# Optimization experiments

Hardware: AMD Instinct MI355X
Metric: run time of the kernel (lower is better)

## Reference

```python
import jax, jax.numpy as jnp
import numpy as np

B, T = 64, 20          # batch, caption length
C, HW = 512, 196       # cnn_channels, width*height (14x14)
V, E, U = 10000, 256, 512  # n_tokens, emb_size, lstm_units
MAX_NORM = 5.0


def setup_inputs() -> dict:
    key = jax.random.key(0)
    ks = jax.random.split(key, 12)
    s = 0.02
    return {
        "image_features": jax.random.normal(ks[0], (B, C, HW), jnp.float32),
        "captions_ix": jax.random.randint(ks[1], (B, T), 0, V, dtype=jnp.int32),
        "W_h0": jax.random.normal(ks[2], (U, C), jnp.float32) * s,
        "b_h0": jnp.zeros((U,), jnp.float32),
        "W_c0": jax.random.normal(ks[3], (U, C), jnp.float32) * s,
        "b_c0": jnp.zeros((U,), jnp.float32),
        "emb": jax.random.normal(ks[4], (V, E), jnp.float32) * s,
        "W_key": jax.random.normal(ks[5], (U, C), jnp.float32) * s,
        "b_key": jnp.zeros((U,), jnp.float32),
        "W_ih": jax.random.normal(ks[6], (4 * U, C + E), jnp.float32) * s,
        "b_ih": jnp.zeros((4 * U,), jnp.float32),
        "W_hh": jax.random.normal(ks[7], (4 * U, U), jnp.float32) * s,
        "b_hh": jnp.zeros((4 * U,), jnp.float32),
        "W_out": jax.random.normal(ks[8], (V, C + E + U), jnp.float32) * s,
        "b_out": jnp.zeros((V,), jnp.float32),
    }


def _caption_net(image_features, captions_ix, W_h0, b_h0, W_c0, b_c0, emb,
                 W_key, b_key, W_ih, b_ih, W_hh, b_hh, W_out, b_out):
    feats_mean = image_features.mean(axis=2)                # [B, C]
    hid0 = feats_mean @ W_h0.T + b_h0                       # [B, U]
    cell0 = feats_mean @ W_c0.T + b_c0                      # [B, U]
    feats = jnp.transpose(image_features, (0, 2, 1))        # [B, HW, C]
    keys = feats @ W_key.T + b_key                          # [B, HW, U]

    # nn.Embedding(max_norm=5): renorm rows whose L2 norm exceeds 5
    norms = jnp.linalg.norm(emb, axis=1, keepdims=True)
    emb_eff = emb * jnp.minimum(1.0, MAX_NORM / jnp.maximum(norms, 1e-12))
    cap_emb = emb_eff[captions_ix]                          # [B, T, E]

    inv_scale = 1.0 / (keys.shape[2] ** 0.5)

    def step(carry, emb_t):
        hid, cell = carry
        # scaled dot-product attention, query = current hidden state
        scores = jnp.einsum('bu,bku->bk', hid, keys) * inv_scale   # [B, HW]
        w = jax.nn.softmax(scores, axis=1)
        a = jnp.einsum('bk,bkc->bc', w, feats)                     # [B, C]
        x = jnp.concatenate([emb_t, a], axis=1)                    # [B, E+C]
        gates = x @ W_ih.T + b_ih + hid @ W_hh.T + b_hh            # [B, 4U]
        i, f, g, o = jnp.split(gates, 4, axis=1)
        cell = jax.nn.sigmoid(f) * cell + jax.nn.sigmoid(i) * jnp.tanh(g)
        hid = jax.nn.sigmoid(o) * jnp.tanh(cell)
        out = jnp.concatenate([hid, a, emb_t], axis=1)             # [B, U+C+E]
        return (hid, cell), (out, w)

    (_, _), (outs, attn) = jax.lax.scan(step, (hid0, cell0),
                                        jnp.transpose(cap_emb, (1, 0, 2)))
    outs = jnp.transpose(outs, (1, 0, 2))                   # [B, T, U+C+E]
    attn = jnp.transpose(attn, (1, 0, 2))                   # [B, T, HW]
    logits = outs @ W_out.T + b_out                         # [B, T, V]
    return logits, attn


def reference(image_features, captions_ix, W_h0, b_h0, W_c0, b_c0, emb,
              W_key, b_key, W_ih, b_ih, W_hh, b_hh, W_out, b_out):
    return _caption_net(image_features, captions_ix, W_h0, b_h0, W_c0, b_c0,
                        emb, W_key, b_key, W_ih, b_ih, W_hh, b_hh, W_out, b_out)
```

## Files before the change

kernel.cpp:

```cpp
#include <hip/hip_runtime.h>
#include <math.h>

#define B 64
#define T 20
#define C 512
#define HW 196
#define V 10000
#define E 256
#define U 512
#define G4U 2048
#define ODIM 1280
#define KTOT 1280
#define NBLK 64

typedef short bf8_t __attribute__((ext_vector_type(8)));
typedef float f4_t  __attribute__((ext_vector_type(4)));

__device__ __forceinline__ unsigned short f2bf(float f) {
    unsigned int u = __float_as_uint(f);
    return (unsigned short)((u + 0x7fffu + ((u >> 16) & 1u)) >> 16);
}
__device__ __forceinline__ float bf2f(unsigned short s) {
    return __uint_as_float((unsigned int)s << 16);
}
__device__ __forceinline__ float bflo(unsigned int kv) { return __uint_as_float(kv << 16); }
__device__ __forceinline__ float bfhi(unsigned int kv) { return __uint_as_float(kv & 0xffff0000u); }

__device__ __forceinline__ void coh_load4x2(const void* p0, const void* p1,
                                            uint4& r0, uint4& r1) {
    asm volatile("global_load_dwordx4 %0, %2, off sc0 sc1\n\t"
                 "global_load_dwordx4 %1, %3, off sc0 sc1\n\t"
                 "s_waitcnt vmcnt(0)"
                 : "=&v"(r0), "=&v"(r1) : "v"(p0), "v"(p1) : "memory");
}
__device__ __forceinline__ void coh_load4_issue(const void* p, uint4& r) {
    asm volatile("global_load_dwordx4 %0, %1, off sc0 sc1"
                 : "=&v"(r) : "v"(p) : "memory");
}
__device__ __forceinline__ void wait_vm0() {
    asm volatile("s_waitcnt vmcnt(0)" ::: "memory");
    __builtin_amdgcn_sched_barrier(0);
}
__device__ __forceinline__ void coh_store1f(void* p, float v) {
    asm volatile("global_store_dword %0, %1, off sc0 sc1" :: "v"(p), "v"(v) : "memory");
}
__device__ __forceinline__ void coh_store1u(void* p, unsigned int v) {
    asm volatile("global_store_dword %0, %1, off sc0 sc1" :: "v"(p), "v"(v) : "memory");
}
__device__ __forceinline__ void coh_store_us(void* p, unsigned int v) {
    asm volatile("global_store_short %0, %1, off sc0 sc1" :: "v"(p), "v"(v) : "memory");
}
__device__ __forceinline__ int coh_load_int(const int* p) {
    int v;
    asm volatile("global_load_dword %0, %1, off sc0 sc1\n\t"
                 "s_waitcnt vmcnt(0)"
                 : "=v"(v) : "v"(p) : "memory");
    return v;
}
__device__ __forceinline__ void coh_store_int(int* p, int v) {
    asm volatile("global_store_dword %0, %1, off sc0 sc1" :: "v"(p), "v"(v) : "memory");
}

__device__ __forceinline__ void gbarf(int* barf, int e) {
    asm volatile("s_waitcnt vmcnt(0)" ::: "memory");
    __syncthreads();
    int tid = threadIdx.x;
    if (blockIdx.x == 0) {
        if (tid == 0) coh_store_int(barf + 16, e);
        if (tid < 64) {
            while (!__all(coh_load_int(barf + 16 + tid * 16) >= e)) {}
            if (tid == 0) coh_store_int(barf, e);
        }
    } else {
        if (tid == 0) {
            coh_store_int(barf + 16 + blockIdx.x * 16, e);
            while (coh_load_int(barf) < e) {}
        }
    }
    __syncthreads();
}

__global__ void k_mean(const float* __restrict__ img, float* __restrict__ fm) {
    int wave = threadIdx.x >> 6;
    int lane = threadIdx.x & 63;
    int row = blockIdx.x * 4 + wave;
    const float* p = img + (size_t)row * HW;
    float s = p[lane] + p[lane + 64] + p[lane + 128];
    if (lane < 4) s += p[lane + 192];
    for (int off = 32; off > 0; off >>= 1) s += __shfl_down(s, off, 64);
    if (lane == 0) fm[row] = s * (1.0f / HW);
}

__global__ void k_init(const float* __restrict__ fm,
                       const float* __restrict__ W_h0, const float* __restrict__ b_h0,
                       const float* __restrict__ W_c0, const float* __restrict__ b_c0,
                       unsigned short* __restrict__ xb, float* __restrict__ cell) {
    int wv = blockIdx.x * 4 + (threadIdx.x >> 6);
    int lane = threadIdx.x & 63;
    int which = wv >> 15;
    int r = wv & 32767;
    int b = r >> 9, u = r & 511;
    const float* W = which ? W_c0 : W_h0;
    const float* bias = which ? b_c0 : b_h0;
    const float* f = fm + b * C;
    const float* w = W + (size_t)u * C;
    float s = 0.f;
    #pragma unroll
    for (int c = 0; c < C; c += 64) s += f[c + lane] * w[c + lane];
    for (int off = 32; off > 0; off >>= 1) s += __shfl_down(s, off, 64);
    if (lane == 0) {
        float v = s + bias[u];
        if (which) cell[r] = v;
        else       xb[(size_t)b * KTOT + 768 + u] = f2bf(v);
    }
}

__global__ void k_wkt(const float* __restrict__ Wk, float* __restrict__ WkT) {
    __shared__ float tile[64][65];
    int u0 = blockIdx.x * 64, c0 = blockIdx.y * 64;
    int x = threadIdx.x & 63, y0 = threadIdx.x >> 6;
    #pragma unroll
    for (int i = 0; i < 16; i++) {
        int r = y0 * 16 + i;
        tile[r][x] = Wk[(size_t)(u0 + r) * C + c0 + x];
    }
    __syncthreads();
    #pragma unroll
    for (int i = 0; i < 16; i++) {
        int r = y0 * 16 + i;
        WkT[(size_t)(c0 + r) * U + u0 + x] = tile[x][r];
    }
}

__global__ __launch_bounds__(256) void k_keys(const float* __restrict__ img,
        const float* __restrict__ WkT, const float* __restrict__ b_key,
        unsigned short* __restrict__ keys2) {
    __shared__ unsigned short st[32][200];
    int b = blockIdx.x >> 4;
    int u0 = (blockIdx.x & 15) * 32;
    int wave = __builtin_amdgcn_readfirstlane(threadIdx.x >> 6);
    int lane = threadIdx.x & 63;
    int lk = lane < 49 ? lane : 48;
    const f4_t* imgb = (const f4_t*)(img + (size_t)b * C * HW);
    f4_t acc[8];
    #pragma unroll
    for (int j = 0; j < 8; j++) acc[j] = (f4_t){0.f, 0.f, 0.f, 0.f};
    const float* wp = WkT + u0 + wave * 8;
    for (int c = 0; c < C; c++) {
        f4_t v = imgb[c * 49 + lk];
        const float* w = wp + (size_t)c * U;
        #pragma unroll
        for (int j = 0; j < 8; j++) acc[j] += v * w[j];
    }
    if (lane < 49) {
        #pragma unroll
        for (int j = 0; j < 8; j++) {
            float bk = b_key[u0 + wave * 8 + j];
            int ul = wave * 8 + j;
            int k = lane * 4;
            st[ul][k + 0] = f2bf(acc[j].x + bk);
            st[ul][k + 1] = f2bf(acc[j].y + bk);
            st[ul][k + 2] = f2bf(acc[j].z + bk);
            st[ul][k + 3] = f2bf(acc[j].w + bk);
        }
    }
    __syncthreads();
    int ui = threadIdx.x & 15;
    int kr = threadIdx.x >> 4;
    #pragma unroll
    for (int pass = 0; pass < 13; pass++) {
        int k = pass * 16 + kr;
        if (k < HW) {
            unsigned int lo = st[ui * 2][k];
            unsigned int hi = st[ui * 2 + 1][k];
            *(unsigned int*)&keys2[((size_t)b * HW + k) * U + u0 + ui * 2] = (hi << 16) | lo;
        }
    }
}

__global__ void k_wg(const float* __restrict__ W_ih, const float* __restrict__ W_hh,
                     unsigned short* __restrict__ Wg) {
    int j = blockIdx.x;
    int tid = threadIdx.x;
    const float* s1 = W_ih + (size_t)j * 768;
    const float* s2 = W_hh + (size_t)j * 512;
    unsigned short* dst = Wg + (size_t)j * KTOT;
    #pragma unroll
    for (int p = 0; p < 3; p++) dst[tid + p * 256] = f2bf(s1[tid + p * 256]);
    #pragma unroll
    for (int p = 0; p < 2; p++) dst[768 + tid + p * 256] = f2bf(s2[tid + p * 256]);
}

__global__ void k_emb(const int* __restrict__ ix, const float* __restrict__ emb,
                      unsigned short* __restrict__ outs, int* __restrict__ barf) {
    int bt = blockIdx.x;
    int e = threadIdx.x;
    if (bt == 0) {
        for (int i = e; i < 1040; i += 256) barf[i] = 0;
    }
    int row = ix[bt];
    float v = emb[(size_t)row * E + e];
    __shared__ float red[4];
    float sq = v * v;
    for (int off = 32; off > 0; off >>= 1) sq += __shfl_down(sq, off, 64);
    int wave = e >> 6, lane = e & 63;
    if (lane == 0) red[wave] = sq;
    __syncthreads();
    float norm = sqrtf(red[0] + red[1] + red[2] + red[3]);
    float scale = fminf(1.0f, 5.0f / fmaxf(norm, 1e-12f));
    outs[(size_t)bt * ODIM + (U + C) + e] = f2bf(v * scale);
}

__global__ __launch_bounds__(256) void k_wo(const float* __restrict__ W,
                                            unsigned short* __restrict__ Wb) {
    size_t i = ((size_t)blockIdx.x * 256 + threadIdx.x) * 8;
    float4 f0 = *(const float4*)(W + i);
    float4 f1 = *(const float4*)(W + i + 4);
    uint4 q;
    q.x = ((unsigned int)f2bf(f0.y) << 16) | f2bf(f0.x);
    q.y = ((unsigned int)f2bf(f0.w) << 16) | f2bf(f0.z);
    q.z = ((unsigned int)f2bf(f1.y) << 16) | f2bf(f1.x);
    q.w = ((unsigned int)f2bf(f1.w) << 16) | f2bf(f1.z);
    *(uint4*)(Wb + i) = q;
}

__global__ __launch_bounds__(256) void k_loop(
    unsigned short* __restrict__ outs, unsigned short* __restrict__ xb,
    const float* __restrict__ cell0, float* __restrict__ gates4,
    const unsigned short* __restrict__ keys2, const float* __restrict__ img,
    const float* __restrict__ b_ih, const float* __restrict__ b_hh,
    const unsigned short* __restrict__ Wg, float* __restrict__ attn,
    int* __restrict__ barf) {
    int b = blockIdx.x;
    int tid = threadIdx.x;
    int wave = __builtin_amdgcn_readfirstlane(tid >> 6);
    int lane = tid & 63;
    int m16 = lane & 15, quad = lane >> 4;
    __shared__ float hidS[U];
    __shared__ float wS[256];
    __shared__ float red[4];
    __shared__ unsigned short As[64 * 320];

    float c_r[2], bsum[2][4];
    #pragma unroll
    for (int p = 0; p < 2; p++) {
        int u = tid + p * 256;
        c_r[p] = cell0[(size_t)b * U + u];
        #pragma unroll
        for (int q = 0; q < 4; q++)
            bsum[p][q] = b_ih[q * 512 + u] + b_hh[q * 512 + u];
    }

    int j0g = blockIdx.x * 32;
    int srow = tid >> 2, scol = tid & 3;
    int arow = wave * 16 + m16;
    int ep = 0;

    for (int t = 0; t <= T; ++t) {
        if (t > 0) {
            const float* g0 = gates4 + (size_t)b * 2048 + tid * 4;
            uint4 r0, r1;
            coh_load4x2(g0, g0 + 1024, r0, r1);
            #pragma unroll
            for (int p = 0; p < 2; p++) {
                int u = tid + p * 256;
                float4 gv = p ? *(float4*)&r1 : *(float4*)&r0;
                float g0f = gv.x + bsum[p][0];
                float g1f = gv.y + bsum[p][1];
                float g2f = gv.z + bsum[p][2];
                float g3f = gv.w + bsum[p][3];
                float si = 1.f / (1.f + expf(-g0f));
                float sf = 1.f / (1.f + expf(-g1f));
                float tg = tanhf(g2f);
                float so = 1.f / (1.f + expf(-g3f));
                float cn = sf * c_r[p] + si * tg;
                c_r[p] = cn;
                float hn = so * tanhf(cn);
                hidS[u] = hn;
                unsigned int hv = f2bf(hn);
                outs[((size_t)b * T + (t - 1)) * ODIM + u] = (unsigned short)hv;
                coh_store_us(&xb[(size_t)b * KTOT + 768 + u], hv);
            }
        } else {
            #pragma unroll
            for (int p = 0; p < 2; p++) {
                int u = tid + p * 256;
                hidS[u] = bf2f(xb[(size_t)b * KTOT + 768 + u]);
            }
        }
        if (t == T) break;
        __syncthreads();

        float sc = 0.f;
        if (tid < HW) {
            const uint4* kr = (const uint4*)(keys2 + ((size_t)b * HW + tid) * U);
            float acc = 0.f;
            #pragma unroll 8
            for (int i = 0; i < 64; i++) {
                uint4 kv = kr[i];
                float4 h0 = *(const float4*)&hidS[i * 8];
                float4 h1 = *(const float4*)&hidS[i * 8 + 4];
                acc += bflo(kv.x) * h0.x + bfhi(kv.x) * h0.y
                     + bflo(kv.y) * h0.z + bfhi(kv.y) * h0.w
                     + bflo(kv.z) * h1.x + bfhi(kv.z) * h1.y
                     + bflo(kv.w) * h1.z + bfhi(kv.w) * h1.w;
            }
            sc = acc * 0.044194173824159216f;
        }
        {
            float v = (tid < HW) ? sc : -1e30f;
            float m = v;
            for (int off = 32; off > 0; off >>= 1) m = fmaxf(m, __shfl_down(m, off, 64));
            if (lane == 0) red[wave] = m;
            __syncthreads();
            m = fmaxf(fmaxf(red[0], red[1]), fmaxf(red[2], red[3]));
            float ex = (tid < HW) ? expf(v - m) : 0.f;
            float ssum = ex;
            for (int off = 32; off > 0; off >>= 1) ssum += __shfl_down(ssum, off, 64);
            __syncthreads();
            if (lane == 0) red[wave] = ssum;
            __syncthreads();
            ssum = red[0] + red[1] + red[2] + red[3];
            float w = ex / ssum;
            wS[tid] = w;
            if (tid < HW) attn[((size_t)b * T + t) * HW + tid] = w;
        }
        __syncthreads();

        {
            const float4* imgb = (const float4*)(img + (size_t)b * C * HW);
            #pragma unroll
            for (int p = 0; p < 2; p++) {
                int c = tid + p * 256;
                const float4* rr4 = imgb + c * 49;
                float acc = 0.f;
                for (int k4 = 0; k4 < 49; k4++) {
                    float4 vv = rr4[k4];
                    acc += wS[4 * k4] * vv.x + wS[4 * k4 + 1] * vv.y
                         + wS[4 * k4 + 2] * vv.z + wS[4 * k4 + 3] * vv.w;
                }
                unsigned int av = f2bf(acc);
                coh_store_us(&xb[(size_t)b * KTOT + 256 + c], av);
                outs[((size_t)b * T + t) * ODIM + U + c] = (unsigned short)av;
            }
        }
        if (tid < 128) {
            const unsigned int* src = (const unsigned int*)(outs + ((size_t)b * T + t) * ODIM);
            unsigned int* dst = (unsigned int*)(xb + (size_t)b * KTOT);
            coh_store1u(&dst[tid], src[512 + tid]);
        }

        ++ep; gbarf(barf, ep);

        {
            f4_t acc2[2];
            acc2[0] = (f4_t){0.f, 0.f, 0.f, 0.f};
            acc2[1] = (f4_t){0.f, 0.f, 0.f, 0.f};
            #pragma unroll 1
            for (int s = 0; s < 4; s++) {
                int kbase = s * 320;
                uint4 ra[10];
                #pragma unroll
                for (int p = 0; p < 10; p++)
                    coh_load4_issue(&xb[(size_t)srow * KTOT + kbase + (scol + 4 * p) * 8], ra[p]);
                wait_vm0();
                #pragma unroll
                for (int p = 0; p < 10; p++) {
                    int chunk = scol + 4 * p;
                    *(uint4*)&As[srow * 320 + ((chunk * 8) ^ ((srow & 7) << 3))] = ra[p];
                }
                __syncthreads();
                #pragma unroll
                for (int c = 0; c < 10; c++) {
                    int kl = c * 32 + quad * 8;
                    bf8_t afr = *(const bf8_t*)&As[arow * 320 + (kl ^ ((m16 & 7) << 3))];
                    int kg = kbase + kl;
                    bf8_t b0 = *(const bf8_t*)&Wg[(size_t)(j0g + m16) * KTOT + kg];
                    bf8_t b1 = *(const bf8_t*)&Wg[(size_t)(j0g + 16 + m16) * KTOT + kg];
                    acc2[0] = __builtin_amdgcn_mfma_f32_16x16x32_bf16(afr, b0, acc2[0], 0, 0, 0);
                    acc2[1] = __builtin_amdgcn_mfma_f32_16x16x32_bf16(afr, b1, acc2[1], 0, 0, 0);
                }
                __syncthreads();
            }
            #pragma unroll
            for (int nt = 0; nt < 2; nt++) {
                int n = j0g + nt * 16 + m16;
                int qq = n >> 9, uu = n & 511;
                #pragma unroll
                for (int rr = 0; rr < 4; rr++) {
                    int bb = wave * 16 + quad * 4 + rr;
                    coh_store1f(&gates4[((size_t)bb * 512 + uu) * 4 + qq], acc2[nt][rr]);
                }
            }
        }

        ++ep; gbarf(barf, ep);
    }
}

__global__ __launch_bounds__(256) void k_logits4(
    const unsigned short* __restrict__ A, const float* __restrict__ Wo,
    const float* __restrict__ bo, float* __restrict__ Cout) {
    __shared__ unsigned short As[128][72];
    __shared__ unsigned short Bs[128][72];
    int n0 = blockIdx.x * 128;
    int m0 = blockIdx.y * 128;
    int tid = threadIdx.x;
    int lane = tid & 63, wv = tid >> 6;
    int mw = (wv >> 1) * 64, nw = (wv & 1) * 64;
    int m16 = lane & 15, quad = lane >> 4;
    int srow = tid >> 1, shalf = tid & 1;

    f4_t acc[4][4];
    #pragma unroll
    for (int i = 0; i < 4; i++)
        #pragma unroll
        for (int j = 0; j < 4; j++)
            acc[i][j] = (f4_t){0.f, 0.f, 0.f, 0.f};

    for (int k0 = 0; k0 < KTOT; k0 += 64) {
        {
            const uint4* ap = (const uint4*)&A[(size_t)(m0 + srow) * KTOT + k0 + shalf * 32];
            uint4 a0 = ap[0], a1 = ap[1], a2 = ap[2], a3 = ap[3];
            uint4* dst = (uint4*)&As[srow][shalf * 32];
            dst[0] = a0; dst[1] = a1; dst[2] = a2; dst[3] = a3;
        }
        {
            int n = n0 + srow;
            uint4 q[4];
            if (n < V) {
                const float4* bp = (const float4*)&Wo[(size_t)n * KTOT + k0 + shalf * 32];
                #pragma unroll
                for (int g = 0; g < 4; g++) {
                    float4 f0 = bp[g * 2], f1 = bp[g * 2 + 1];
                    q[g].x = ((unsigned int)f2bf(f0.y) << 16) | f2bf(f0.x);
                    q[g].y = ((unsigned int)f2bf(f0.w) << 16) | f2bf(f0.z);
                    q[g].z = ((unsigned int)f2bf(f1.y) << 16) | f2bf(f1.x);
                    q[g].w = ((unsigned int)f2bf(f1.w) << 16) | f2bf(f1.z);
                }
            } else {
                #pragma unroll
                for (int g = 0; g < 4; g++) q[g] = (uint4){0u, 0u, 0u, 0u};
            }
            uint4* dst = (uint4*)&Bs[srow][shalf * 32];
            #pragma unroll
            for (int g = 0; g < 4; g++) dst[g] = q[g];
        }
        __syncthreads();
        #pragma unroll
        for (int h = 0; h < 2; h++) {
            bf8_t af[4], bf[4];
            #pragma unroll
            for (int i = 0; i < 4; i++)
                af[i] = *(const bf8_t*)&As[mw + i * 16 + m16][h * 32 + quad * 8];
            #pragma unroll
            for (int j = 0; j < 4; j++)
                bf[j] = *(const bf8_t*)&Bs[nw + j * 16 + m16][h * 32 + quad * 8];
            #pragma unroll
            for (int i = 0; i < 4; i++)
                #pragma unroll
                for (int j = 0; j < 4; j++)
                    acc[i][j] = __builtin_amdgcn_mfma_f32_16x16x32_bf16(af[i], bf[j], acc[i][j], 0, 0, 0);
        }
        __syncthreads();
    }

    #pragma unroll
    for (int j = 0; j < 4; j++) {
        int n = n0 + nw + j * 16 + m16;
        if (n >= V) continue;
        float bias = bo[n];
        #pragma unroll
        for (int i = 0; i < 4; i++) {
            int mb = m0 + mw + i * 16 + quad * 4;
            #pragma unroll
            for (int r = 0; r < 4; r++)
                Cout[(size_t)(mb + r) * V + n] = acc[i][j][r] + bias;
        }
    }
}

__global__ __launch_bounds__(256) void k_logits5(
    const unsigned short* __restrict__ A, const unsigned short* __restrict__ Wob,
    const float* __restrict__ bo, float* __restrict__ Cout) {
    __shared__ unsigned short As[128][72];
    __shared__ unsigned short Bs[128][72];
    int n0 = blockIdx.x * 128;
    int m0 = blockIdx.y * 128;
    int tid = threadIdx.x;
    int lane = tid & 63, wv = tid >> 6;
    int mw = (wv >> 1) * 64, nw = (wv & 1) * 64;
    int m16 = lane & 15, quad = lane >> 4;
    int srow = tid >> 1, shalf = tid & 1;

    f4_t acc[4][4];
    #pragma unroll
    for (int i = 0; i < 4; i++)
        #pragma unroll
        for (int j = 0; j < 4; j++)
            acc[i][j] = (f4_t){0.f, 0.f, 0.f, 0.f};

    for (int k0 = 0; k0 < KTOT; k0 += 64) {
        {
            const uint4* ap = (const uint4*)&A[(size_t)(m0 + srow) * KTOT + k0 + shalf * 32];
            uint4 a0 = ap[0], a1 = ap[1], a2 = ap[2], a3 = ap[3];
            uint4* dst = (uint4*)&As[srow][shalf * 32];
            dst[0] = a0; dst[1] = a1; dst[2] = a2; dst[3] = a3;
        }
        {
            int n = n0 + srow;
            uint4 q[4];
            if (n < V) {
                const uint4* bp = (const uint4*)&Wob[(size_t)n * KTOT + k0 + shalf * 32];
                #pragma unroll
                for (int g = 0; g < 4; g++) q[g] = bp[g];
            } else {
                #pragma unroll
                for (int g = 0; g < 4; g++) q[g] = (uint4){0u, 0u, 0u, 0u};
            }
            uint4* dst = (uint4*)&Bs[srow][shalf * 32];
            #pragma unroll
            for (int g = 0; g < 4; g++) dst[g] = q[g];
        }
        __syncthreads();
        #pragma unroll
        for (int h = 0; h < 2; h++) {
            bf8_t af[4], bf[4];
            #pragma unroll
            for (int i = 0; i < 4; i++)
                af[i] = *(const bf8_t*)&As[mw + i * 16 + m16][h * 32 + quad * 8];
            #pragma unroll
            for (int j = 0; j < 4; j++)
                bf[j] = *(const bf8_t*)&Bs[nw + j * 16 + m16][h * 32 + quad * 8];
            #pragma unroll
            for (int i = 0; i < 4; i++)
                #pragma unroll
                for (int j = 0; j < 4; j++)
                    acc[i][j] = __builtin_amdgcn_mfma_f32_16x16x32_bf16(af[i], bf[j], acc[i][j], 0, 0, 0);
        }
        __syncthreads();
    }

    #pragma unroll
    for (int j = 0; j < 4; j++) {
        int n = n0 + nw + j * 16 + m16;
        if (n >= V) continue;
        float bias = bo[n];
        #pragma unroll
        for (int i = 0; i < 4; i++) {
            int mb = m0 + mw + i * 16 + quad * 4;
            #pragma unroll
            for (int r = 0; r < 4; r++)
                Cout[(size_t)(mb + r) * V + n] = acc[i][j][r] + bias;
        }
    }
}

extern "C" void kernel_launch(void* const* d_in, const int* in_sizes, int n_in,
                              void* d_out, int out_size, void* d_ws, size_t ws_size,
                              hipStream_t stream) {
    const float* img   = (const float*)d_in[0];
    const int*   capix = (const int*)d_in[1];
    const float* W_h0  = (const float*)d_in[2];
    const float* b_h0  = (const float*)d_in[3];
    const float* W_c0  = (const float*)d_in[4];
    const float* b_c0  = (const float*)d_in[5];
    const float* emb   = (const float*)d_in[6];
    const float* W_key = (const float*)d_in[7];
    const float* b_key = (const float*)d_in[8];
    const float* W_ih  = (const float*)d_in[9];
    const float* b_ih  = (const float*)d_in[10];
    const float* W_hh  = (const float*)d_in[11];
    const float* b_hh  = (const float*)d_in[12];
    const float* W_out = (const float*)d_in[13];
    const float* b_out = (const float*)d_in[14];

    float* ws = (float*)d_ws;
    float* gates4    = ws;
    float* fm        = ws;
    float* cell      = gates4 + 131072;
    float* WkT       = cell + 32768;
    int*   barf      = (int*)WkT;
    unsigned short* Wg    = (unsigned short*)(WkT + 262144);
    unsigned short* xb    = Wg + 2621440;
    unsigned short* outs  = xb + 81920;
    unsigned short* keys2 = outs + (size_t)B * T * ODIM;
    const size_t WOB_OFF = 23232576;
    unsigned short* Wob = (unsigned short*)((char*)d_ws + WOB_OFF);
    bool use_wob = ws_size >= WOB_OFF + (size_t)V * KTOT * 2;

    float* logits = (float*)d_out;
    float* attn   = logits + (size_t)B * T * V;

    k_mean<<<(B * C) / 4, 256, 0, stream>>>(img, fm);
    k_init<<<(2 * B * U) / 4, 256, 0, stream>>>(fm, W_h0, b_h0, W_c0, b_c0, xb, cell);
    k_wkt<<<dim3(8, 8), 256, 0, stream>>>(W_key, WkT);
    k_keys<<<B * 16, 256, 0, stream>>>(img, WkT, b_key, keys2);
    k_wg<<<G4U, 256, 0, stream>>>(W_ih, W_hh, Wg);
    k_emb<<<B * T, 256, 0, stream>>>(capix, emb, outs, barf);
    if (use_wob)
        k_wo<<<(V * KTOT) / 2048, 256, 0, stream>>>(W_out, Wob);

    k_loop<<<NBLK, 256, 0, stream>>>(outs, xb, cell, gates4, keys2, img,
                                     b_ih, b_hh, Wg, attn, barf);

    if (use_wob)
        k_logits5<<<dim3((V + 127) / 128, (B * T) / 128), 256, 0, stream>>>(outs, Wob, b_out, logits);
    else
        k_logits4<<<dim3((V + 127) / 128, (B * T) / 128), 256, 0, stream>>>(outs, W_out, b_out, logits);
}
```

Baseline: 1.243 ms.

## Double loop-kernel block size and precompute fp16 image features for attention context

Doubles the recurrent loop kernel to 512 threads per block so each thread handles one hidden unit, one context channel and one 16x16 MFMA tile instead of two. Adds a pre-pass that converts image features to padded fp16 rows so the attention-weighted context sum can use packed fp16 dot instructions over half-size data. The aim is to shorten each serial timestep by spreading work across more waves and cutting memory traffic in the context reduction. In exchange it adds fp16 rounding to the context vector, an extra conversion kernel, more workspace, and possibly lower occupancy or register headroom.

```diff
diff --git a/kernel.cpp b/kernel.cpp
--- a/kernel.cpp
+++ b/kernel.cpp
@@ -15,6 +15,7 @@
 
 typedef short bf8_t __attribute__((ext_vector_type(8)));
 typedef float f4_t  __attribute__((ext_vector_type(4)));
+typedef _Float16 h2_t __attribute__((ext_vector_type(2)));
 
 __device__ __forceinline__ unsigned short f2bf(float f) {
     unsigned int u = __float_as_uint(f);
@@ -25,13 +26,15 @@
 }
 __device__ __forceinline__ float bflo(unsigned int kv) { return __uint_as_float(kv << 16); }
 __device__ __forceinline__ float bfhi(unsigned int kv) { return __uint_as_float(kv & 0xffff0000u); }
-
-__device__ __forceinline__ void coh_load4x2(const void* p0, const void* p1,
-                                            uint4& r0, uint4& r1) {
-    asm volatile("global_load_dwordx4 %0, %2, off sc0 sc1\n\t"
-                 "global_load_dwordx4 %1, %3, off sc0 sc1\n\t"
+__device__ __forceinline__ unsigned short f2h(float f) {
+    _Float16 h = (_Float16)f;
+    return *(unsigned short*)&h;
+}
+
+__device__ __forceinline__ void coh_load4w(const void* p, uint4& r) {
+    asm volatile("global_load_dwordx4 %0, %1, off sc0 sc1\n\t"
                  "s_waitcnt vmcnt(0)"
-                 : "=&v"(r0), "=&v"(r1) : "v"(p0), "v"(p1) : "memory");
+                 : "=&v"(r) : "v"(p) : "memory");
 }
 __device__ __forceinline__ void coh_load4_issue(const void* p, uint4& r) {
     asm volatile("global_load_dwordx4 %0, %1, off sc0 sc1"
@@ -211,6 +214,21 @@
     outs[(size_t)bt * ODIM + (U + C) + e] = f2bf(v * scale);
 }
 
+__global__ __launch_bounds__(256) void k_img(const float* __restrict__ img,
+                                             unsigned short* __restrict__ img2) {
+    int oid = blockIdx.x * 256 + threadIdx.x;
+    int row = oid / 25, p = oid - row * 25;
+    const float* src = img + (size_t)row * HW;
+    unsigned short h[8];
+    #pragma unroll
+    for (int i = 0; i < 8; i++) {
+        int k = p * 8 + i;
+        float f = (k < HW) ? src[k] : 0.f;
+        h[i] = f2h(f);
+    }
+    *(uint4*)&img2[(size_t)row * 200 + p * 8] = *(const uint4*)h;
+}
+
 __global__ __launch_bounds__(256) void k_wo(const float* __restrict__ W,
                                             unsigned short* __restrict__ Wb) {
     size_t i = ((size_t)blockIdx.x * 256 + threadIdx.x) * 8;
@@ -224,10 +242,11 @@
     *(uint4*)(Wb + i) = q;
 }
 
-__global__ __launch_bounds__(256) void k_loop(
+__global__ __launch_bounds__(512) void k_loop(
     unsigned short* __restrict__ outs, unsigned short* __restrict__ xb,
     const float* __restrict__ cell0, float* __restrict__ gates4,
     const unsigned short* __restrict__ keys2, const float* __restrict__ img,
+    const unsigned short* __restrict__ img2,
     const float* __restrict__ b_ih, const float* __restrict__ b_hh,
     const unsigned short* __restrict__ Wg, float* __restrict__ attn,
     int* __restrict__ barf) {
@@ -237,56 +256,45 @@
     int lane = tid & 63;
     int m16 = lane & 15, quad = lane >> 4;
     __shared__ float hidS[U];
-    __shared__ float wS[256];
-    __shared__ float red[4];
+    __shared__ float wS[200];
+    __shared__ float red[8];
+    __shared__ __align__(16) unsigned int wH[100];
     __shared__ unsigned short As[64 * 320];
 
-    float c_r[2], bsum[2][4];
-    #pragma unroll
-    for (int p = 0; p < 2; p++) {
-        int u = tid + p * 256;
-        c_r[p] = cell0[(size_t)b * U + u];
-        #pragma unroll
-        for (int q = 0; q < 4; q++)
-            bsum[p][q] = b_ih[q * 512 + u] + b_hh[q * 512 + u];
-    }
-
-    int j0g = blockIdx.x * 32;
-    int srow = tid >> 2, scol = tid & 3;
-    int arow = wave * 16 + m16;
+    float c_r = cell0[(size_t)b * U + tid];
+    float bsum[4];
+    #pragma unroll
+    for (int q = 0; q < 4; q++)
+        bsum[q] = b_ih[q * 512 + tid] + b_hh[q * 512 + tid];
+
+    int j0g = b * 32;
+    int mt = wave >> 1, nt = wave & 1;
+    int arow = mt * 16 + m16;
+    int srow = tid >> 3, sc8 = tid & 7;
     int ep = 0;
 
     for (int t = 0; t <= T; ++t) {
         if (t > 0) {
-            const float* g0 = gates4 + (size_t)b * 2048 + tid * 4;
-            uint4 r0, r1;
-            coh_load4x2(g0, g0 + 1024, r0, r1);
-            #pragma unroll
-            for (int p = 0; p < 2; p++) {
-                int u = tid + p * 256;
-                float4 gv = p ? *(float4*)&r1 : *(float4*)&r0;
-                float g0f = gv.x + bsum[p][0];
-                float g1f = gv.y + bsum[p][1];
-                float g2f = gv.z + bsum[p][2];
-                float g3f = gv.w + bsum[p][3];
-                float si = 1.f / (1.f + expf(-g0f));
-                float sf = 1.f / (1.f + expf(-g1f));
-                float tg = tanhf(g2f);
-                float so = 1.f / (1.f + expf(-g3f));
-                float cn = sf * c_r[p] + si * tg;
-                c_r[p] = cn;
-                float hn = so * tanhf(cn);
-                hidS[u] = hn;
-                unsigned int hv = f2bf(hn);
-                outs[((size_t)b * T + (t - 1)) * ODIM + u] = (unsigned short)hv;
-                coh_store_us(&xb[(size_t)b * KTOT + 768 + u], hv);
-            }
+            uint4 r0;
+            coh_load4w(gates4 + ((size_t)b * 512 + tid) * 4, r0);
+            float4 gv = *(float4*)&r0;
+            float g0f = gv.x + bsum[0];
+            float g1f = gv.y + bsum[1];
+            float g2f = gv.z + bsum[2];
+            float g3f = gv.w + bsum[3];
+            float si = 1.f / (1.f + expf(-g0f));
+            float sf = 1.f / (1.f + expf(-g1f));
+            float tg = tanhf(g2f);
+            float so = 1.f / (1.f + expf(-g3f));
+            float cn = sf * c_r + si * tg;
+            c_r = cn;
+            float hn = so * tanhf(cn);
+            hidS[tid] = hn;
+            unsigned int hv = f2bf(hn);
+            outs[((size_t)b * T + (t - 1)) * ODIM + tid] = (unsigned short)hv;
+            coh_store_us(&xb[(size_t)b * KTOT + 768 + tid], hv);
         } else {
-            #pragma unroll
-            for (int p = 0; p < 2; p++) {
-                int u = tid + p * 256;
-                hidS[u] = bf2f(xb[(size_t)b * KTOT + 768 + u]);
-            }
+            hidS[tid] = bf2f(xb[(size_t)b * KTOT + 768 + tid]);
         }
         if (t == T) break;
         __syncthreads();
@@ -313,36 +321,69 @@
             for (int off = 32; off > 0; off >>= 1) m = fmaxf(m, __shfl_down(m, off, 64));
             if (lane == 0) red[wave] = m;
             __syncthreads();
-            m = fmaxf(fmaxf(red[0], red[1]), fmaxf(red[2], red[3]));
+            m = red[0];
+            #pragma unroll
+            for (int i = 1; i < 8; i++) m = fmaxf(m, red[i]);
             float ex = (tid < HW) ? expf(v - m) : 0.f;
             float ssum = ex;
             for (int off = 32; off > 0; off >>= 1) ssum += __shfl_down(ssum, off, 64);
             __syncthreads();
             if (lane == 0) red[wave] = ssum;
             __syncthreads();
-            ssum = red[0] + red[1] + red[2] + red[3];
+            ssum = red[0];
+            #pragma unroll
+            for (int i = 1; i < 8; i++) ssum += red[i];
             float w = ex / ssum;
-            wS[tid] = w;
-            if (tid < HW) attn[((size_t)b * T + t) * HW + tid] = w;
+            if (tid < HW) {
+                wS[tid] = w;
+                attn[((size_t)b * T + t) * HW + tid] = w;
+            } else if (tid < 200) {
+                wS[tid] = 0.f;
+            }
         }
         __syncthreads();
+        if (tid < 100) {
+            unsigned int lo = f2h(wS[2 * tid]);
+            unsigned int hi = f2h(wS[2 * tid + 1]);
+            wH[tid] = (hi << 16) | lo;
+        }
+        __syncthreads();
 
         {
-            const float4* imgb = (const float4*)(img + (size_t)b * C * HW);
-            #pragma unroll
-            for (int p = 0; p < 2; p++) {
-                int c = tid + p * 256;
-                const float4* rr4 = imgb + c * 49;
-                float acc = 0.f;
+            float acc = 0.f;
+            if (img2) {
+                const uint4* rowp = (const uint4*)(img2 + ((size_t)b * 512 + tid) * 200);
+                const uint4* w4 = (const uint4*)wH;
+                #pragma unroll
+                for (int p = 0; p < 25; p++) {
+                    uint4 v = rowp[p];
+                    uint4 wv = w4[p];
+                    const h2_t* va = (const h2_t*)&v;
+                    const h2_t* wa = (const h2_t*)&wv;
+#if __has_builtin(__builtin_amdgcn_fdot2)
+                    acc = __builtin_amdgcn_fdot2(va[0], wa[0], acc, false);
+                    acc = __builtin_amdgcn_fdot2(va[1], wa[1], acc, false);
+                    acc = __builtin_amdgcn_fdot2(va[2], wa[2], acc, false);
+                    acc = __builtin_amdgcn_fdot2(va[3], wa[3], acc, false);
+#else
+                    #pragma unroll
+                    for (int q = 0; q < 4; q++) {
+                        acc += (float)va[q][0] * (float)wa[q][0];
+                        acc += (float)va[q][1] * (float)wa[q][1];
+                    }
+#endif
+                }
+            } else {
+                const float4* rr4 = (const float4*)(img + (size_t)b * C * HW) + tid * 49;
                 for (int k4 = 0; k4 < 49; k4++) {
                     float4 vv = rr4[k4];
                     acc += wS[4 * k4] * vv.x + wS[4 * k4 + 1] * vv.y
                          + wS[4 * k4 + 2] * vv.z + wS[4 * k4 + 3] * vv.w;
                 }
-                unsigned int av = f2bf(acc);
-                coh_store_us(&xb[(size_t)b * KTOT + 256 + c], av);
-                outs[((size_t)b * T + t) * ODIM + U + c] = (unsigned short)av;
             }
+            unsigned int av = f2bf(acc);
+            coh_store_us(&xb[(size_t)b * KTOT + 256 + tid], av);
+            outs[((size_t)b * T + t) * ODIM + U + tid] = (unsigned short)av;
         }
         if (tid < 128) {
             const unsigned int* src = (const unsigned int*)(outs + ((size_t)b * T + t) * ODIM);
@@ -353,44 +394,39 @@
         ++ep; gbarf(barf, ep);
 
         {
-            f4_t acc2[2];
-            acc2[0] = (f4_t){0.f, 0.f, 0.f, 0.f};
-            acc2[1] = (f4_t){0.f, 0.f, 0.f, 0.f};
+            f4_t acc2 = (f4_t){0.f, 0.f, 0.f, 0.f};
             #pragma unroll 1
             for (int s = 0; s < 4; s++) {
                 int kbase = s * 320;
-                uint4 ra[10];
-                #pragma unroll
-                for (int p = 0; p < 10; p++)
-                    coh_load4_issue(&xb[(size_t)srow * KTOT + kbase + (scol + 4 * p) * 8], ra[p]);
+                uint4 ra[5];
+                #pragma unroll
+                for (int p = 0; p < 5; p++) {
+                    int chunk = sc8 + 8 * p;
+                    coh_load4_issue(&xb[(size_t)srow * KTOT + kbase + chunk * 8], ra[p]);
+                }
                 wait_vm0();
                 #pragma unroll
-                for (int p = 0; p < 10; p++) {
-                    int chunk = scol + 4 * p;
+                for (int p = 0; p < 5; p++) {
+                    int chunk = sc8 + 8 * p;
                     *(uint4*)&As[srow * 320 + ((chunk * 8) ^ ((srow & 7) << 3))] = ra[p];
                 }
                 __syncthreads();
                 #pragma unroll
                 for (int c = 0; c < 10; c++) {
                     int kl = c * 32 + quad * 8;
-                    bf8_t afr = *(const bf8_t*)&As[arow * 320 + (kl ^ ((m16 & 7) << 3))];
+                    bf8_t afr = *(const bf8_t*)&As[arow * 320 + (kl ^ ((arow & 7) << 3))];
                     int kg = kbase + kl;
-                    bf8_t b0 = *(const bf8_t*)&Wg[(size_t)(j0g + m16) * KTOT + kg];
-                    bf8_t b1 = *(const bf8_t*)&Wg[(size_t)(j0g + 16 + m16) * KTOT + kg];
-                    acc2[0] = __builtin_amdgcn_mfma_f32_16x16x32_bf16(afr, b0, acc2[0], 0, 0, 0);
-                    acc2[1] = __builtin_amdgcn_mfma_f32_16x16x32_bf16(afr, b1, acc2[1], 0, 0, 0);
+                    bf8_t bfr = *(const bf8_t*)&Wg[(size_t)(j0g + nt * 16 + m16) * KTOT + kg];
+                    acc2 = __builtin_amdgcn_mfma_f32_16x16x32_bf16(afr, bfr, acc2, 0, 0, 0);
                 }
                 __syncthreads();
             }
-            #pragma unroll
-            for (int nt = 0; nt < 2; nt++) {
-                int n = j0g + nt * 16 + m16;
-                int qq = n >> 9, uu = n & 511;
-                #pragma unroll
-                for (int rr = 0; rr < 4; rr++) {
-                    int bb = wave * 16 + quad * 4 + rr;
-                    coh_store1f(&gates4[((size_t)bb * 512 + uu) * 4 + qq], acc2[nt][rr]);
-                }
+            int n = j0g + nt * 16 + m16;
+            int qq = n >> 9, uu = n & 511;
+            #pragma unroll
+            for (int rr = 0; rr < 4; rr++) {
+                int bb = mt * 16 + quad * 4 + rr;
+                coh_store1f(&gates4[((size_t)bb * 512 + uu) * 4 + qq], acc2[rr]);
             }
         }
 
@@ -585,7 +621,10 @@
     unsigned short* xb    = Wg + 2621440;
     unsigned short* outs  = xb + 81920;
     unsigned short* keys2 = outs + (size_t)B * T * ODIM;
-    const size_t WOB_OFF = 23232576;
+    const size_t IMG2_OFF = 23232576;
+    unsigned short* img2 = (unsigned short*)((char*)d_ws + IMG2_OFF);
+    bool use_img2 = ws_size >= IMG2_OFF + (size_t)B * C * 200 * 2;
+    const size_t WOB_OFF = 36339776;
     unsigned short* Wob = (unsigned short*)((char*)d_ws + WOB_OFF);
     bool use_wob = ws_size >= WOB_OFF + (size_t)V * KTOT * 2;
 
@@ -598,10 +637,13 @@
     k_keys<<<B * 16, 256, 0, stream>>>(img, WkT, b_key, keys2);
     k_wg<<<G4U, 256, 0, stream>>>(W_ih, W_hh, Wg);
     k_emb<<<B * T, 256, 0, stream>>>(capix, emb, outs, barf);
+    if (use_img2)
+        k_img<<<3200, 256, 0, stream>>>(img, img2);
     if (use_wob)
         k_wo<<<(V * KTOT) / 2048, 256, 0, stream>>>(W_out, Wob);
 
-    k_loop<<<NBLK, 256, 0, stream>>>(outs, xb, cell, gates4, keys2, img,
+    k_loop<<<NBLK, 512, 0, stream>>>(outs, xb, cell, gates4, keys2, img,
+                                     use_img2 ? img2 : (const unsigned short*)nullptr,
                                      b_ih, b_hh, Wg, attn, barf);
 
     if (use_wob)
```

Result: faster. 1.179 ms (-5.1%).
